# Kernel tuning notes

Hardware: AMD Instinct MI355X
Metric: run time of the kernel (lower is better)

The kernel has to match this reference:

```python
import jax, jax.numpy as jnp
import numpy as np

D_MODEL = 1024
NHEAD = 16
DK = D_MODEL // NHEAD  # 64
B, S = 2, 2048


def setup_inputs() -> dict:
    key = jax.random.key(0)
    ks = jax.random.split(key, 8)
    Q = jax.random.normal(ks[0], (B, S, D_MODEL), dtype=jnp.float32)
    K = jax.random.normal(ks[1], (B, S, D_MODEL), dtype=jnp.float32)
    V = jax.random.normal(ks[2], (B, S, D_MODEL), dtype=jnp.float32)
    additive_mask = jax.random.normal(ks[3], (S, S), dtype=jnp.float32)
    key_padding_mask = jnp.zeros((B, S), dtype=jnp.int32)  # ignored by the module
    # Per-head projection weights, stacked over heads: [H, d_model, dk]
    scale = 1.0 / np.sqrt(D_MODEL)
    WQ = jax.random.normal(ks[4], (NHEAD, D_MODEL, DK), dtype=jnp.float32) * scale
    WK = jax.random.normal(ks[5], (NHEAD, D_MODEL, DK), dtype=jnp.float32) * scale
    WV = jax.random.normal(ks[6], (NHEAD, D_MODEL, DK), dtype=jnp.float32) * scale
    WO = jax.random.normal(ks[7], (D_MODEL, D_MODEL), dtype=jnp.float32) * scale
    return {"Q": Q, "K": K, "V": V, "additive_mask": additive_mask,
            "key_padding_mask": key_padding_mask,
            "WQ": WQ, "WK": WK, "WV": WV, "WO": WO}


def reference(Q, K, V, additive_mask, key_padding_mask, WQ, WK, WV, WO):
    # Per-head projections, batched over heads: [B, H, S, dk]
    q = jnp.einsum('bsd,hdk->bhsk', Q, WQ)
    k = jnp.einsum('bsd,hdk->bhsk', K, WK)
    v = jnp.einsum('bsd,hdk->bhsk', V, WV)
    # scores: [B, H, S, S]; mask broadcasts over batch and head
    scores = jnp.einsum('bhqk,bhsk->bhqs', q, k) / np.sqrt(DK)
    scores = scores + additive_mask[None, None, :, :]
    attn = jax.nn.softmax(scores, axis=-1)
    o = jnp.einsum('bhqs,bhsk->bhqk', attn, v)  # [B, H, S, dk]
    # concat heads in head order == transpose + reshape to [B, S, H*dk]
    o = o.transpose(0, 2, 1, 3).reshape(Q.shape[0], Q.shape[1], D_MODEL)
    return o @ WO
```

## Files before the change

### kernel.cpp

```cpp
#include <hip/hip_runtime.h>
#include <hip/hip_bf16.h>
#include <stdint.h>

#define D_MODEL 1024
#define NHEAD 16
#define DKH 64
#define BATCH 2
#define SEQ 2048
#define LOG2E 1.44269504088896f

typedef __bf16 bf16_t;
typedef __bf16 bf16x8 __attribute__((ext_vector_type(8)));
typedef float f32x4 __attribute__((ext_vector_type(4)));
typedef float f32x16 __attribute__((ext_vector_type(16)));

__device__ __forceinline__ float fast_exp2(float x) {
#if __has_builtin(__builtin_amdgcn_exp2f)
  return __builtin_amdgcn_exp2f(x);
#else
  return exp2f(x);
#endif
}

__device__ __forceinline__ void gload_lds16(const bf16_t* g, bf16_t* l) {
  auto gp = (const __attribute__((address_space(1))) void*)(uintptr_t)g;
  auto lp = (__attribute__((address_space(3))) void*)(uintptr_t)l;
  __builtin_amdgcn_global_load_lds(gp, lp, 16, 0, 0);
}

__device__ __forceinline__ uint32_t pkbf(float lo, float hi) {
  bf16_t a = (bf16_t)lo, c = (bf16_t)hi;
  uint16_t ua, uc;
  __builtin_memcpy(&ua, &a, 2);
  __builtin_memcpy(&uc, &c, 2);
  return (uint32_t)ua | ((uint32_t)uc << 16);
}

__device__ __forceinline__ void perm32swap(uint32_t& a, uint32_t& b) {
  asm volatile("v_permlane32_swap_b32 %0, %1" : "+v"(a), "+v"(b));
}

__global__ void k_cvtw(const float* __restrict__ WQ, const float* __restrict__ WK,
                       const float* __restrict__ WV, const float* __restrict__ WO,
                       bf16_t* __restrict__ wt) {
  int j = blockIdx.x * 256 + threadIdx.x;
  int d = j & 1023, n = j >> 10;
  if (n < 3072) {
    int proj = n >> 10, h = (n >> 6) & 15, k = n & 63;
    const float* w = proj == 0 ? WQ : (proj == 1 ? WK : WV);
    float scale = proj == 0 ? (0.125f * LOG2E) : 1.0f;
    wt[j] = (bf16_t)(w[(h << 16) + (d << 6) + k] * scale);
  } else {
    wt[j] = (bf16_t)WO[(d << 10) + (n - 3072)];
  }
}

__global__ void k_maskg(const float* __restrict__ M, bf16_t* __restrict__ Mf) {
  int t = blockIdx.x * 256 + threadIdx.x;
  int wch = t & 7, lane = (t >> 3) & 63;
  int kvt = (t >> 9) & 31, qt = t >> 14;
  int h = lane >> 5, ql = lane & 31;
  int q = qt * 32 + ql;
  int t32 = wch >> 2, r2 = wch & 3;
  int kvb = kvt * 64 + t32 * 32 + 8 * r2 + 4 * h;
  float4 m4 = *reinterpret_cast<const float4*>(M + (size_t)q * SEQ + kvb);
  bf16_t o[4];
  o[0] = (bf16_t)(m4.x * LOG2E); o[1] = (bf16_t)(m4.y * LOG2E);
  o[2] = (bf16_t)(m4.z * LOG2E); o[3] = (bf16_t)(m4.w * LOG2E);
  *reinterpret_cast<ushort4*>(Mf + (size_t)t * 4) = *reinterpret_cast<ushort4*>(o);
}

__global__ __launch_bounds__(256)
void k_gemm_qkv(const float* __restrict__ Qs, const float* __restrict__ Ks32,
                const float* __restrict__ Vs32, const bf16_t* __restrict__ Bt,
                bf16_t* __restrict__ qh, bf16_t* __restrict__ Kf,
                bf16_t* __restrict__ Vf) {
  __shared__ __align__(16) bf16_t As[128 * 32];
  __shared__ __align__(16) bf16_t Bs[128 * 32];
  const int tid = threadIdx.x;
  const int lane = tid & 63, wave = tid >> 6;
  const int g = lane >> 4, lr = lane & 15;
  const int bm = blockIdx.x, bn = blockIdx.y;
  const int pn = bn >> 3;
  const float* Ap32 = pn == 0 ? Qs : (pn == 1 ? Ks32 : Vs32);
  const int wm = (wave >> 1) << 6, wn = (wave & 1) << 6;
  const int arow = tid >> 1, ako = (tid & 1) << 4;
  const float* aptr = Ap32 + (size_t)(bm * 128 + arow) * 1024 + ako;
  f32x4 acc[4][4] = {};

  float4 fA0 = *reinterpret_cast<const float4*>(aptr);
  float4 fA1 = *reinterpret_cast<const float4*>(aptr + 4);
  float4 fA2 = *reinterpret_cast<const float4*>(aptr + 8);
  float4 fA3 = *reinterpret_cast<const float4*>(aptr + 12);

  for (int kt = 0; kt < 1024; kt += 32) {
#pragma unroll
    for (int cc = 0; cc < 2; cc++) {
      int c = tid + cc * 256;
      int row = c >> 2, ko = (c & 3) << 3;
      gload_lds16(Bt + (size_t)(bn * 128 + row) * 1024 + kt + ko, Bs + c * 8);
    }
    {
      bf16x8 o0, o1;
      o0[0] = (bf16_t)fA0.x; o0[1] = (bf16_t)fA0.y; o0[2] = (bf16_t)fA0.z; o0[3] = (bf16_t)fA0.w;
      o0[4] = (bf16_t)fA1.x; o0[5] = (bf16_t)fA1.y; o0[6] = (bf16_t)fA1.z; o0[7] = (bf16_t)fA1.w;
      o1[0] = (bf16_t)fA2.x; o1[1] = (bf16_t)fA2.y; o1[2] = (bf16_t)fA2.z; o1[3] = (bf16_t)fA2.w;
      o1[4] = (bf16_t)fA3.x; o1[5] = (bf16_t)fA3.y; o1[6] = (bf16_t)fA3.z; o1[7] = (bf16_t)fA3.w;
      *reinterpret_cast<bf16x8*>(As + arow * 32 + ako) = o0;
      *reinterpret_cast<bf16x8*>(As + arow * 32 + ako + 8) = o1;
    }
    if (kt + 32 < 1024) {
      const float* np = aptr + kt + 32;
      fA0 = *reinterpret_cast<const float4*>(np);
      fA1 = *reinterpret_cast<const float4*>(np + 4);
      fA2 = *reinterpret_cast<const float4*>(np + 8);
      fA3 = *reinterpret_cast<const float4*>(np + 12);
    }
    __syncthreads();
    bf16x8 af[4], bfr[4];
#pragma unroll
    for (int t = 0; t < 4; t++)
      af[t] = *reinterpret_cast<const bf16x8*>(As + (wm + t * 16 + lr) * 32 + g * 8);
#pragma unroll
    for (int t = 0; t < 4; t++)
      bfr[t] = *reinterpret_cast<const bf16x8*>(Bs + (wn + t * 16 + lr) * 32 + g * 8);
    __builtin_amdgcn_s_setprio(1);
#pragma unroll
    for (int i = 0; i < 4; i++)
#pragma unroll
      for (int j = 0; j < 4; j++)
        acc[i][j] = __builtin_amdgcn_mfma_f32_16x16x32_bf16(af[i], bfr[j], acc[i][j], 0, 0, 0);
    __builtin_amdgcn_s_setprio(0);
    __syncthreads();
  }

#pragma unroll
  for (int i = 0; i < 4; i++)
#pragma unroll
    for (int j = 0; j < 4; j++)
#pragma unroll
      for (int e = 0; e < 4; e++) {
        int row = (bm << 7) + wm + i * 16 + g * 4 + e;
        int col = ((bn & 7) << 7) + wn + j * 16 + lr;
        float v = acc[i][j][e];
        int b = row >> 11, s = row & 2047, h = col >> 6, d = col & 63;
        size_t bh32 = (size_t)((b << 4) + h) * 32;
        if (pn == 0) {
          qh[((size_t)(((b << 4) + h) * SEQ + s) << 6) + d] = (bf16_t)v;
        } else if (pn == 1) {
          int kt2 = s >> 6, u = s & 63, t32 = u >> 5, ql2 = u & 31;
          int kk2 = d >> 4, hq2 = (d >> 3) & 1, e2 = d & 7;
          Kf[(bh32 + kt2) * 4096 + (t32 * 4 + kk2) * 512 + (hq2 * 32 + ql2) * 8 + e2] = (bf16_t)v;
        } else {
          int kt2 = s >> 6, u = s & 63, s2 = u >> 4, hq2 = (u >> 3) & 1, e2 = u & 7;
          int dkt = d >> 5, ql2 = d & 31;
          Vf[(bh32 + kt2) * 4096 + (dkt * 4 + s2) * 512 + (hq2 * 32 + ql2) * 8 + e2] = (bf16_t)v;
        }
      }
}

__global__ __launch_bounds__(256)
void k_gemm_wo(const bf16_t* __restrict__ A, const bf16_t* __restrict__ Bt,
               float* __restrict__ C) {
  __shared__ __align__(16) bf16_t As[64 * 32];
  __shared__ __align__(16) bf16_t Bs[128 * 32];
  const int tid = threadIdx.x;
  const int lane = tid & 63, wave = tid >> 6;
  const int g = lane >> 4, lr = lane & 15;
  const int bm = blockIdx.x, bn = blockIdx.y;
  const int wm = (wave >> 1) << 5, wn = (wave & 1) << 6;
  f32x4 acc[2][4] = {};

  for (int kt = 0; kt < 1024; kt += 32) {
    {
      int row = tid >> 2, ko = (tid & 3) << 3;
      gload_lds16(A + (size_t)(bm * 64 + row) * 1024 + kt + ko, As + tid * 8);
    }
#pragma unroll
    for (int cc = 0; cc < 2; cc++) {
      int c = tid + cc * 256;
      int row = c >> 2, ko = (c & 3) << 3;
      gload_lds16(Bt + (size_t)(bn * 128 + row) * 1024 + kt + ko, Bs + c * 8);
    }
    __syncthreads();
    bf16x8 af[2], bfr[4];
#pragma unroll
    for (int t = 0; t < 2; t++)
      af[t] = *reinterpret_cast<const bf16x8*>(As + (wm + t * 16 + lr) * 32 + g * 8);
#pragma unroll
    for (int t = 0; t < 4; t++)
      bfr[t] = *reinterpret_cast<const bf16x8*>(Bs + (wn + t * 16 + lr) * 32 + g * 8);
    __builtin_amdgcn_s_setprio(1);
#pragma unroll
    for (int i = 0; i < 2; i++)
#pragma unroll
      for (int j = 0; j < 4; j++)
        acc[i][j] = __builtin_amdgcn_mfma_f32_16x16x32_bf16(af[i], bfr[j], acc[i][j], 0, 0, 0);
    __builtin_amdgcn_s_setprio(0);
    __syncthreads();
  }
#pragma unroll
  for (int i = 0; i < 2; i++)
#pragma unroll
    for (int j = 0; j < 4; j++)
#pragma unroll
      for (int e = 0; e < 4; e++) {
        int row = (bm << 6) + wm + i * 16 + g * 4 + e;
        int col = (bn << 7) + wn + j * 16 + lr;
        C[(size_t)row * D_MODEL + col] = acc[i][j][e];
      }
}

__global__ __launch_bounds__(512, 4)
void k_attn6(const bf16_t* __restrict__ Qh, const bf16_t* __restrict__ Kf,
             const bf16_t* __restrict__ Vf, const bf16_t* __restrict__ Mf,
             bf16_t* __restrict__ O) {
  __shared__ __align__(16) bf16_t Ks[2][2][4096];
  __shared__ __align__(16) bf16_t Vs[2][2][4096];
  const int bh = blockIdx.y, b = bh >> 4, h = bh & 15;
  const int tid = threadIdx.x, w = tid >> 6, lane = tid & 63;
  const int qw = w & 3, hh = w >> 2;
  const int hq = lane >> 5, ql = lane & 31;
  const int tid256 = tid & 255;
  const int qbase = blockIdx.x * 128 + qw * 32;
  const bf16_t* qp = Qh + (size_t)bh * SEQ * DKH;
  const bf16_t* kfp = Kf + (size_t)bh * 32 * 4096;
  const bf16_t* vfp = Vf + (size_t)bh * 32 * 4096;
  const int qt = blockIdx.x * 4 + qw;
  const bf16_t* mp = Mf + ((size_t)(qt * 32 + hh * 16) * 64 + lane) * 32;
  const int NIT = 16;

  bf16x8 aq[4];
#pragma unroll
  for (int kk = 0; kk < 4; kk++)
    aq[kk] = *reinterpret_cast<const bf16x8*>(
        qp + (size_t)(qbase + ql) * DKH + kk * 16 + hq * 8);

  f32x16 oacc[2] = {};
  f32x16 lacc = {};
  const bf16_t onev = (bf16_t)1.0f;
  const bf16x8 ones = {onev, onev, onev, onev, onev, onev, onev, onev};

  auto stage = [&](int buf, int kt) {
#pragma unroll
    for (int cc = 0; cc < 2; cc++) {
      int c = tid256 + cc * 256;
      gload_lds16(kfp + (size_t)kt * 4096 + c * 8, &Ks[hh][buf][c * 8]);
      gload_lds16(vfp + (size_t)kt * 4096 + c * 8, &Vs[hh][buf][c * 8]);
    }
  };

  stage(0, hh * 16);
  bf16x8 mv[4];
#pragma unroll
  for (int j = 0; j < 4; j++)
    mv[j] = *reinterpret_cast<const bf16x8*>(mp + j * 8);
  __syncthreads();

  for (int it = 0; it < NIT; ++it) {
    const int cur = it & 1;
    if (it + 1 < NIT) stage(cur ^ 1, hh * 16 + it + 1);

    const bf16_t* kb = Ks[hh][cur];
    const bf16_t* vb = Vs[hh][cur];

    f32x16 p[2];
#pragma unroll
    for (int t32 = 0; t32 < 2; t32++) {
      f32x16 a = {};
      __builtin_amdgcn_s_setprio(1);
#pragma unroll
      for (int kk = 0; kk < 4; kk++) {
        bf16x8 bk = *reinterpret_cast<const bf16x8*>(kb + (t32 * 4 + kk) * 512 + lane * 8);
        a = __builtin_amdgcn_mfma_f32_32x32x16_bf16(bk, aq[kk], a, 0, 0, 0);
      }
      __builtin_amdgcn_s_setprio(0);
      p[t32] = a;
    }

    bf16x8 paf[4];
#pragma unroll
    for (int s = 0; s < 4; s++) {
      const int t32 = s >> 1, rb = (s & 1) * 8;
      float pes[8];
#pragma unroll
      for (int j = 0; j < 8; j++) {
        int v = t32 * 16 + rb + j;
        float x = p[t32][rb + j] + (float)mv[v >> 3][v & 7];
        pes[j] = fast_exp2(x);
      }
      uint32_t u0 = pkbf(pes[0], pes[1]), u1 = pkbf(pes[2], pes[3]);
      uint32_t w0 = pkbf(pes[4], pes[5]), w1 = pkbf(pes[6], pes[7]);
      perm32swap(u0, w0);
      perm32swap(u1, w1);
      union { uint32_t wd[4]; bf16x8 v8; } fu;
      fu.wd[0] = u0; fu.wd[1] = u1; fu.wd[2] = w0; fu.wd[3] = w1;
      paf[s] = fu.v8;
      lacc = __builtin_amdgcn_mfma_f32_32x32x16_bf16(paf[s], ones, lacc, 0, 0, 0);
    }

    {
      const bf16_t* mn = mp + (size_t)((it + 1 < NIT) ? (it + 1) : it) * 2048;
#pragma unroll
      for (int j = 0; j < 4; j++)
        mv[j] = *reinterpret_cast<const bf16x8*>(mn + j * 8);
    }

#pragma unroll
    for (int dkt = 0; dkt < 2; dkt++) {
      __builtin_amdgcn_s_setprio(1);
#pragma unroll
      for (int s = 0; s < 4; s++) {
        bf16x8 bv = *reinterpret_cast<const bf16x8*>(vb + (dkt * 4 + s) * 512 + lane * 8);
        oacc[dkt] = __builtin_amdgcn_mfma_f32_32x32x16_bf16(paf[s], bv, oacc[dkt], 0, 0, 0);
      }
      __builtin_amdgcn_s_setprio(0);
    }
    __syncthreads();
  }

  float* smO = (float*)&Ks[0][0][0];
  float* smL = (float*)&Vs[0][0][0];
  if (w >= 4) {
    int base = (qw * 64 + lane) * 32;
#pragma unroll
    for (int dkt = 0; dkt < 2; dkt++)
#pragma unroll
      for (int cg = 0; cg < 4; cg++) {
        int chs = ((dkt * 4 + cg) ^ (lane & 7)) * 4;
        float4 val = {oacc[dkt][cg * 4], oacc[dkt][cg * 4 + 1],
                      oacc[dkt][cg * 4 + 2], oacc[dkt][cg * 4 + 3]};
        *reinterpret_cast<float4*>(&smO[base + chs]) = val;
      }
    int lb = (qw * 64 + lane) * 16;
#pragma unroll
    for (int cg = 0; cg < 4; cg++) {
      int chs = (cg ^ (lane & 3)) * 4;
      float4 lv = {lacc[cg * 4], lacc[cg * 4 + 1], lacc[cg * 4 + 2], lacc[cg * 4 + 3]};
      *reinterpret_cast<float4*>(&smL[lb + chs]) = lv;
    }
  }
  __syncthreads();
  if (w < 4) {
    int base = (qw * 64 + lane) * 32;
#pragma unroll
    for (int dkt = 0; dkt < 2; dkt++)
#pragma unroll
      for (int cg = 0; cg < 4; cg++) {
        int chs = ((dkt * 4 + cg) ^ (lane & 7)) * 4;
        float4 pv = *reinterpret_cast<const float4*>(&smO[base + chs]);
#pragma unroll
        for (int e = 0; e < 4; e++) oacc[dkt][cg * 4 + e] += pv[e];
      }
    int lb = (qw * 64 + lane) * 16;
#pragma unroll
    for (int cg = 0; cg < 4; cg++) {
      int chs = (cg ^ (lane & 3)) * 4;
      float4 lv = *reinterpret_cast<const float4*>(&smL[lb + chs]);
      lacc[cg * 4] += lv.x; lacc[cg * 4 + 1] += lv.y;
      lacc[cg * 4 + 2] += lv.z; lacc[cg * 4 + 3] += lv.w;
    }
    float inv[16];
#pragma unroll
    for (int reg = 0; reg < 16; reg++) inv[reg] = 1.0f / lacc[reg];
#pragma unroll
    for (int dkt = 0; dkt < 2; dkt++)
#pragma unroll
      for (int reg = 0; reg < 16; reg++) {
        int qrow = (reg & 3) + 8 * (reg >> 2) + 4 * hq;
        float v = oacc[dkt][reg] * inv[reg];
        O[(size_t)(b * SEQ + qbase + qrow) * D_MODEL + (h << 6) + dkt * 32 + ql] = (bf16_t)v;
      }
  }
}

extern "C" void kernel_launch(void* const* d_in, const int* in_sizes, int n_in,
                              void* d_out, int out_size, void* d_ws, size_t ws_size,
                              hipStream_t stream) {
  const float* Q  = (const float*)d_in[0];
  const float* K  = (const float*)d_in[1];
  const float* V  = (const float*)d_in[2];
  const float* M  = (const float*)d_in[3];
  const float* WQ = (const float*)d_in[5];
  const float* WK = (const float*)d_in[6];
  const float* WV = (const float*)d_in[7];
  const float* WO = (const float*)d_in[8];

  char* ws = (char*)d_ws;
  const size_t MB = 1 << 20;
  bf16_t* Mf    = (bf16_t*)(ws + 24 * MB);
  bf16_t* WqkvT = (bf16_t*)(ws + 32 * MB);
  bf16_t* WoT   = (bf16_t*)(ws + 38 * MB);
  bf16_t* qh    = (bf16_t*)(ws + 40 * MB);
  bf16_t* Kf    = (bf16_t*)(ws + 48 * MB);
  bf16_t* Vf    = (bf16_t*)(ws + 56 * MB);
  bf16_t* Ob    = (bf16_t*)(ws + 64 * MB);

  k_maskg<<<4096, 256, 0, stream>>>(M, Mf);
  k_cvtw<<<16384, 256, 0, stream>>>(WQ, WK, WV, WO, WqkvT);

  k_gemm_qkv<<<dim3(32, 24), 256, 0, stream>>>(Q, K, V, WqkvT, qh, Kf, Vf);

  k_attn6<<<dim3(16, 32), 512, 0, stream>>>(qh, Kf, Vf, Mf, Ob);

  k_gemm_wo<<<dim3(64, 8), 256, 0, stream>>>(Ob, WoT, (float*)d_out);
}
```

Baseline: 159.4 us.

## Replace MFMA row-sum with scalar accumulation and remap attention blocks to XCDs

The softmax denominator was computed with an extra MFMA against a ones vector. It is now accumulated as a per-lane scalar sum of the exponentials, and the half-wave partials are combined with shuffles at the end. The attention grid is also flattened to 1D and remapped so that blocks sharing a batch-head land on the same XCD, which should improve L2 reuse of K/V. The risk is extra VALU adds and shuffles in the epilogue, and a correctness dependence on the lane-to-row mapping.

Measured after the change: 150.0 us. -5.9%, faster.

```diff
diff --git a/kernel.cpp b/kernel.cpp
--- a/kernel.cpp
+++ b/kernel.cpp
@@ -217,16 +217,20 @@
              bf16_t* __restrict__ O) {
   __shared__ __align__(16) bf16_t Ks[2][2][4096];
   __shared__ __align__(16) bf16_t Vs[2][2][4096];
-  const int bh = blockIdx.y, b = bh >> 4, h = bh & 15;
+  const int bid = blockIdx.x;
+  const int xcd = bid & 7, loc = bid >> 3;
+  const int bh = xcd * 4 + (loc >> 4);
+  const int qtile = loc & 15;
+  const int b = bh >> 4, h = bh & 15;
   const int tid = threadIdx.x, w = tid >> 6, lane = tid & 63;
   const int qw = w & 3, hh = w >> 2;
   const int hq = lane >> 5, ql = lane & 31;
   const int tid256 = tid & 255;
-  const int qbase = blockIdx.x * 128 + qw * 32;
+  const int qbase = qtile * 128 + qw * 32;
   const bf16_t* qp = Qh + (size_t)bh * SEQ * DKH;
   const bf16_t* kfp = Kf + (size_t)bh * 32 * 4096;
   const bf16_t* vfp = Vf + (size_t)bh * 32 * 4096;
-  const int qt = blockIdx.x * 4 + qw;
+  const int qt = qtile * 4 + qw;
   const bf16_t* mp = Mf + ((size_t)(qt * 32 + hh * 16) * 64 + lane) * 32;
   const int NIT = 16;
 
@@ -237,9 +241,7 @@
         qp + (size_t)(qbase + ql) * DKH + kk * 16 + hq * 8);
 
   f32x16 oacc[2] = {};
-  f32x16 lacc = {};
-  const bf16_t onev = (bf16_t)1.0f;
-  const bf16x8 ones = {onev, onev, onev, onev, onev, onev, onev, onev};
+  float lsum = 0.f;
 
   auto stage = [&](int buf, int kt) {
 #pragma unroll
@@ -287,7 +289,9 @@
       for (int j = 0; j < 8; j++) {
         int v = t32 * 16 + rb + j;
         float x = p[t32][rb + j] + (float)mv[v >> 3][v & 7];
-        pes[j] = fast_exp2(x);
+        float pe = fast_exp2(x);
+        lsum += pe;
+        pes[j] = pe;
       }
       uint32_t u0 = pkbf(pes[0], pes[1]), u1 = pkbf(pes[2], pes[3]);
       uint32_t w0 = pkbf(pes[4], pes[5]), w1 = pkbf(pes[6], pes[7]);
@@ -296,7 +300,6 @@
       union { uint32_t wd[4]; bf16x8 v8; } fu;
       fu.wd[0] = u0; fu.wd[1] = u1; fu.wd[2] = w0; fu.wd[3] = w1;
       paf[s] = fu.v8;
-      lacc = __builtin_amdgcn_mfma_f32_32x32x16_bf16(paf[s], ones, lacc, 0, 0, 0);
     }
 
     {
@@ -332,13 +335,7 @@
                       oacc[dkt][cg * 4 + 2], oacc[dkt][cg * 4 + 3]};
         *reinterpret_cast<float4*>(&smO[base + chs]) = val;
       }
-    int lb = (qw * 64 + lane) * 16;
-#pragma unroll
-    for (int cg = 0; cg < 4; cg++) {
-      int chs = (cg ^ (lane & 3)) * 4;
-      float4 lv = {lacc[cg * 4], lacc[cg * 4 + 1], lacc[cg * 4 + 2], lacc[cg * 4 + 3]};
-      *reinterpret_cast<float4*>(&smL[lb + chs]) = lv;
-    }
+    smL[qw * 64 + lane] = lsum;
   }
   __syncthreads();
   if (w < 4) {
@@ -352,17 +349,14 @@
 #pragma unroll
         for (int e = 0; e < 4; e++) oacc[dkt][cg * 4 + e] += pv[e];
       }
-    int lb = (qw * 64 + lane) * 16;
-#pragma unroll
-    for (int cg = 0; cg < 4; cg++) {
-      int chs = (cg ^ (lane & 3)) * 4;
-      float4 lv = *reinterpret_cast<const float4*>(&smL[lb + chs]);
-      lacc[cg * 4] += lv.x; lacc[cg * 4 + 1] += lv.y;
-      lacc[cg * 4 + 2] += lv.z; lacc[cg * 4 + 3] += lv.w;
-    }
+    lsum += smL[qw * 64 + lane];
+    float lf = lsum + __shfl_xor(lsum, 32);
     float inv[16];
 #pragma unroll
-    for (int reg = 0; reg < 16; reg++) inv[reg] = 1.0f / lacc[reg];
+    for (int reg = 0; reg < 16; reg++) {
+      int qrow = (reg & 3) + 8 * (reg >> 2) + 4 * hq;
+      inv[reg] = 1.0f / __shfl(lf, qrow);
+    }
 #pragma unroll
     for (int dkt = 0; dkt < 2; dkt++)
 #pragma unroll
@@ -401,7 +395,7 @@
 
   k_gemm_qkv<<<dim3(32, 24), 256, 0, stream>>>(Q, K, V, WqkvT, qh, Kf, Vf);
 
-  k_attn6<<<dim3(16, 32), 512, 0, stream>>>(qh, Kf, Vf, Mf, Ob);
+  k_attn6<<<512, 512, 0, stream>>>(qh, Kf, Vf, Mf, Ob);
 
   k_gemm_wo<<<dim3(64, 8), 256, 0, stream>>>(Ob, WoT, (float*)d_out);
 }
```
